# Optimization experiments

Hardware: AMD Instinct MI355X
Metric: run time of the kernel (lower is better)

Reference implementation:

```python
import jax, jax.numpy as jnp
import numpy as np

B = 131072   # batch
D = 16       # input_dim
L1 = 4       # num lattices in layer 1 (= ceil(D / DPL))
DPL = 4      # input_dim_per_lattice
E = 24       # output_size (ensemble columns)
K = 16       # calibrator keypoints per feature
NV = 2 ** DPL  # hypercube corners per lattice (lattice_keypoints=2 per dim)


def setup_inputs() -> dict:
    key = jax.random.key(0)
    k1, k2, k3, k4, k5 = jax.random.split(key, 5)
    x = jax.random.normal(k1, (B, D), jnp.float32)
    # piecewise-linear calibrators: sorted input keypoints, monotone outputs in [0,1]
    cal_kp = jnp.sort(jax.random.uniform(k2, (D, K), jnp.float32, -3.0, 3.0), axis=-1)
    raw = jax.random.uniform(k3, (D, K), jnp.float32, 0.1, 1.0)
    cv = jnp.cumsum(raw, axis=-1)
    cal_vals = (cv - cv[:, :1]) / (cv[:, -1:] - cv[:, :1])  # [D,K] in [0,1], increasing
    kernels1 = jax.random.uniform(k4, (E, L1, NV), jnp.float32)  # per-column layer-1 lattice vertices
    kernels2 = jax.random.uniform(k5, (E, 1, NV), jnp.float32)   # per-column layer-2 lattice vertices
    return {"x": x, "cal_kp": cal_kp, "cal_vals": cal_vals,
            "kernels1": kernels1, "kernels2": kernels2}


def _mlin_weights(xg):
    """Multilinear (HYPERCUBE) interpolation weights for unit lattices.
    xg: [..., L, d] with entries in [0,1]. Returns [..., L, 2^d] corner weights,
    corner index with dim 0 as most-significant bit."""
    d = xg.shape[-1]
    w = jnp.ones(xg.shape[:-1] + (1,), xg.dtype)
    for i in range(d):
        xi = xg[..., i]                              # [..., L]
        pair = jnp.stack([1.0 - xi, xi], axis=-1)    # [..., L, 2]
        w = (w[..., :, None] * pair[..., None, :]).reshape(*xg.shape[:-1], -1)
    return w


def reference(x, cal_kp, cal_vals, kernels1, kernels2):
    # 1) calibrate_and_stack: per-feature piecewise-linear calibration to [0,1]
    xc = jax.vmap(jnp.interp)(x.T, cal_kp, cal_vals).T           # [B, D]
    # 2) layer 1: split D dims into L1 lattices of DPL dims each (clip_inputs=True)
    xg1 = jnp.clip(xc.reshape(-1, L1, DPL), 0.0, 1.0)            # [B, L1, DPL]
    w1 = _mlin_weights(xg1)                                      # [B, L1, 2^DPL]
    h1 = jnp.einsum('blk,elk->ebl', w1, kernels1)                # [E, B, L1]
    # 3) layer 2: one lattice of DPL dims per ensemble column
    xg2 = jnp.clip(h1[:, :, None, :], 0.0, 1.0)                  # [E, B, 1, DPL]
    w2 = _mlin_weights(xg2)                                      # [E, B, 1, 2^DPL]
    out = jnp.einsum('eblk,elk->be', w2, kernels2)               # [B, E]
    return out
```

## Files before the change

### kernel.cpp

```cpp
#include <hip/hip_runtime.h>


typedef _Float16 f16x4 __attribute__((ext_vector_type(4)));
typedef float f32x4 __attribute__((ext_vector_type(4)));
typedef float f32x2 __attribute__((ext_vector_type(2)));

namespace {
constexpr int kD = 16, kE = 24, kK = 16, kNV = 16;
constexpr int kThreads = 256;
constexpr int kRPB = 64;
constexpr int kK2S = 20;
}

static __device__ __forceinline__ f32x2 fma2(f32x2 a, f32x2 b, f32x2 c) {
#if __has_builtin(__builtin_elementwise_fma)
    return __builtin_elementwise_fma(a, b, c);
#else
    return (f32x2){fmaf(a[0], b[0], c[0]), fmaf(a[1], b[1], c[1])};
#endif
}
static __device__ __forceinline__ f32x2 fma2s(f32x2 a, float b, float c) {
    return fma2(a, (f32x2){b, b}, (f32x2){c, c});
}
static __device__ __forceinline__ f32x2 clamp01(f32x2 v) {
#if __has_builtin(__builtin_elementwise_max) && __has_builtin(__builtin_elementwise_min)
    return __builtin_elementwise_min(
        __builtin_elementwise_max(v, (f32x2){0.f, 0.f}), (f32x2){1.f, 1.f});
#else
    return (f32x2){fminf(fmaxf(v[0], 0.f), 1.f), fminf(fmaxf(v[1], 0.f), 1.f)};
#endif
}

__global__ __launch_bounds__(kThreads, 5) void lattice_fwd(
    const float* __restrict__ x,
    const float* __restrict__ cal_kp,
    const float* __restrict__ cal_vals,
    const float* __restrict__ k1,
    const float* __restrict__ k2,
    float* __restrict__ out)
{
    __shared__ float sKp[kD * 16];
    __shared__ f32x4 sEnt[kD * 16];
    __shared__ f16x4 sW[4 * 4 * 64];
    __shared__ f16x4 sK1[4 * 2 * 64];
    __shared__ float sK2[32 * kK2S];

    const int tid  = threadIdx.x;
    const int lane = tid & 63;
    const int wv   = __builtin_amdgcn_readfirstlane(tid >> 6);
    const int q    = lane >> 4;
    const int r15  = lane & 15;

    const int rowBase = blockIdx.x * kRPB + wv * 16;

    f32x4 xin = *reinterpret_cast<const f32x4*>(
        x + (size_t)(rowBase + r15) * kD + 4 * q);

    sKp[tid] = ((tid & 15) == 15) ? __builtin_inff() : cal_kp[tid];
    if (tid < kD * 15) {
        int d = tid / 15;
        int k = tid - d * 15;
        float kp0 = cal_kp[d * kK + k];
        float kp1 = cal_kp[d * kK + k + 1];
        float v0  = cal_vals[d * kK + k];
        float v1  = cal_vals[d * kK + k + 1];
        float dxv = kp1 - kp0;
        float slope = (dxv > 0.0f) ? (v1 - v0) / dxv : 0.0f;
        sEnt[d * 16 + k] = (f32x4){kp0, slope, v0, 0.0f};
    }
    #pragma unroll
    for (int s0 = 0; s0 < 2; ++s0) {
        int s  = tid + s0 * kThreads;
        int l  = s >> 7;
        int n  = (s >> 6) & 1;
        int ls = s & 63;
        int e  = n * 16 + (ls & 15);
        int g  = ls >> 4;
        f16x4 v = {(_Float16)0.f, (_Float16)0.f, (_Float16)0.f, (_Float16)0.f};
        if (e < kE) {
            const float* src = k1 + ((size_t)(e * 4 + l) * kNV + 4 * g);
            v[0] = (_Float16)src[0]; v[1] = (_Float16)src[1];
            v[2] = (_Float16)src[2]; v[3] = (_Float16)src[3];
        }
        sK1[s] = v;
    }
    {
        int e = tid >> 3, j = tid & 7;
        float lo = 0.f, hi = 0.f;
        if (e < kE) { lo = k2[e * kNV + 2 * j]; hi = k2[e * kNV + 2 * j + 1]; }
        sK2[e * kK2S + j]     = lo;
        sK2[e * kK2S + 8 + j] = hi - lo;
    }

    __syncthreads();

    float xc[4];
    #pragma unroll
    for (int i = 0; i < 4; ++i) {
        const int d = 4 * q + i;
        const float xv = xin[i];
        const float* kpb = &sKp[d * 16];
        int j = 0;
        #pragma unroll
        for (int s = 8; s >= 1; s >>= 1) {
            float kps = kpb[j + s];
            j = (xv >= kps) ? j + s : j;
        }
        f32x4 ent = sEnt[d * 16 + j];
        float t = fmaf(ent[1], xv - ent[0], ent[2]);
        xc[i] = fminf(fmaxf(t, 0.0f), 1.0f);
    }

    float wf[16];
    {
        float a = xc[0], b = xc[1], c = xc[2], d = xc[3];
        float t2[2] = {1.0f - a, a};
        float t4[4];
        #pragma unroll
        for (int j = 0; j < 2; ++j) { t4[2*j] = t2[j]*(1.0f-b); t4[2*j+1] = t2[j]*b; }
        float t8[8];
        #pragma unroll
        for (int j = 0; j < 4; ++j) { t8[2*j] = t4[j]*(1.0f-c); t8[2*j+1] = t4[j]*c; }
        #pragma unroll
        for (int j = 0; j < 8; ++j) { wf[2*j] = t8[j]*(1.0f-d); wf[2*j+1] = t8[j]*d; }
    }

    #pragma unroll
    for (int g = 0; g < 4; ++g) {
        f16x4 v;
        v[0] = (_Float16)wf[4*g+0]; v[1] = (_Float16)wf[4*g+1];
        v[2] = (_Float16)wf[4*g+2]; v[3] = (_Float16)wf[4*g+3];
        sW[(wv * 4 + q) * 64 + r15 + 16 * g] = v;
    }
    asm volatile("s_waitcnt lgkmcnt(0)" ::: "memory");

    f16x4 af[4];
    #pragma unroll
    for (int l = 0; l < 4; ++l) af[l] = sW[(wv * 4 + l) * 64 + lane];

    #pragma unroll
    for (int n = 0; n < 2; ++n) {
        const int e = n * 16 + r15;

        f16x4 bf[4];
        #pragma unroll
        for (int l = 0; l < 4; ++l) bf[l] = sK1[(l * 2 + n) * 64 + lane];

        const float* kr = &sK2[e * kK2S];
        f32x4 ke0 = *reinterpret_cast<const f32x4*>(kr);
        f32x4 ke1 = *reinterpret_cast<const f32x4*>(kr + 4);
        f32x4 kd0 = *reinterpret_cast<const f32x4*>(kr + 8);
        f32x4 kd1 = *reinterpret_cast<const f32x4*>(kr + 12);
        float kbe[8] = {ke0[0],ke0[1],ke0[2],ke0[3], ke1[0],ke1[1],ke1[2],ke1[3]};
        float db [8] = {kd0[0],kd0[1],kd0[2],kd0[3], kd1[0],kd1[1],kd1[2],kd1[3]};

        f32x4 acc[4];
        #pragma unroll
        for (int l = 0; l < 4; ++l)
            acc[l] = __builtin_amdgcn_mfma_f32_16x16x16f16(
                af[l], bf[l], (f32x4){0.f, 0.f, 0.f, 0.f}, 0, 0, 0);

        #pragma unroll
        for (int p = 0; p < 2; ++p) {
            f32x2 h0 = clamp01((f32x2){acc[0][2*p], acc[0][2*p+1]});
            f32x2 h1 = clamp01((f32x2){acc[1][2*p], acc[1][2*p+1]});
            f32x2 h2 = clamp01((f32x2){acc[2][2*p], acc[2][2*p+1]});
            f32x2 h3 = clamp01((f32x2){acc[3][2*p], acc[3][2*p+1]});
            f32x2 v8[8];
            #pragma unroll
            for (int j = 0; j < 8; ++j) v8[j] = fma2s(h3, db[j], kbe[j]);
            f32x2 v4[4];
            #pragma unroll
            for (int j = 0; j < 4; ++j) v4[j] = fma2(h2, v8[2*j+1]-v8[2*j], v8[2*j]);
            f32x2 v2[2];
            #pragma unroll
            for (int j = 0; j < 2; ++j) v2[j] = fma2(h1, v4[2*j+1]-v4[2*j], v4[2*j]);
            f32x2 o = fma2(h0, v2[1]-v2[0], v2[0]);
            if (e < kE) {
                size_t r0 = (size_t)(rowBase + q * 4 + 2 * p);
                out[r0 * kE + e]       = o[0];
                out[(r0 + 1) * kE + e] = o[1];
            }
        }
    }
}

extern "C" void kernel_launch(void* const* d_in, const int* in_sizes, int n_in,
                              void* d_out, int out_size, void* d_ws, size_t ws_size,
                              hipStream_t stream) {
    const float* x        = (const float*)d_in[0];
    const float* cal_kp   = (const float*)d_in[1];
    const float* cal_vals = (const float*)d_in[2];
    const float* k1       = (const float*)d_in[3];
    const float* k2       = (const float*)d_in[4];
    float* out = (float*)d_out;

    hipLaunchKernelGGL(lattice_fwd, dim3(131072 / kRPB), dim3(kThreads), 0, stream,
                       x, cal_kp, cal_vals, k1, k2, out);
}
```

Baseline: 14.23 us.

## Pad shared arrays, precompute calibrator affine terms, and reorder layer-2 evaluation to cut registers

Pads the shared keypoint, calibration and weight arrays to odd strides so LDS accesses hit fewer bank conflicts. Each calibrator segment is stored as a slope/intercept pair, so the lookup needs one FMA and a smaller LDS read. The layer-2 kernel table is interleaved and consumed four entries at a time, streaming K2 loads instead of holding all 16 values. Launch bounds go from 5 to 8 blocks per SM, which caps register use to raise occupancy and may cause spills.

```diff
diff --git a/kernel.cpp b/kernel.cpp
--- a/kernel.cpp
+++ b/kernel.cpp
@@ -9,7 +9,10 @@
 constexpr int kD = 16, kE = 24, kK = 16, kNV = 16;
 constexpr int kThreads = 256;
 constexpr int kRPB = 64;
-constexpr int kK2S = 20;
+constexpr int kKpS  = 17;
+constexpr int kAffS = 17;
+constexpr int kWS   = 67;
+constexpr int kK2S  = 20;
 }
 
 static __device__ __forceinline__ f32x2 fma2(f32x2 a, f32x2 b, f32x2 c) {
@@ -23,15 +26,10 @@
     return fma2(a, (f32x2){b, b}, (f32x2){c, c});
 }
 static __device__ __forceinline__ f32x2 clamp01(f32x2 v) {
-#if __has_builtin(__builtin_elementwise_max) && __has_builtin(__builtin_elementwise_min)
-    return __builtin_elementwise_min(
-        __builtin_elementwise_max(v, (f32x2){0.f, 0.f}), (f32x2){1.f, 1.f});
-#else
     return (f32x2){fminf(fmaxf(v[0], 0.f), 1.f), fminf(fmaxf(v[1], 0.f), 1.f)};
-#endif
-}
-
-__global__ __launch_bounds__(kThreads, 5) void lattice_fwd(
+}
+
+__global__ __launch_bounds__(kThreads, 8) void lattice_fwd(
     const float* __restrict__ x,
     const float* __restrict__ cal_kp,
     const float* __restrict__ cal_vals,
@@ -39,9 +37,9 @@
     const float* __restrict__ k2,
     float* __restrict__ out)
 {
-    __shared__ float sKp[kD * 16];
-    __shared__ f32x4 sEnt[kD * 16];
-    __shared__ f16x4 sW[4 * 4 * 64];
+    __shared__ float sKp[kD * kKpS];
+    __shared__ f32x2 sAff[kD * kAffS];
+    __shared__ f16x4 sW[16 * kWS];
     __shared__ f16x4 sK1[4 * 2 * 64];
     __shared__ float sK2[32 * kK2S];
 
@@ -56,7 +54,10 @@
     f32x4 xin = *reinterpret_cast<const f32x4*>(
         x + (size_t)(rowBase + r15) * kD + 4 * q);
 
-    sKp[tid] = ((tid & 15) == 15) ? __builtin_inff() : cal_kp[tid];
+    {
+        int d = tid >> 4, k = tid & 15;
+        sKp[d * kKpS + k] = (k == 15) ? __builtin_inff() : cal_kp[tid];
+    }
     if (tid < kD * 15) {
         int d = tid / 15;
         int k = tid - d * 15;
@@ -66,7 +67,7 @@
         float v1  = cal_vals[d * kK + k + 1];
         float dxv = kp1 - kp0;
         float slope = (dxv > 0.0f) ? (v1 - v0) / dxv : 0.0f;
-        sEnt[d * 16 + k] = (f32x4){kp0, slope, v0, 0.0f};
+        sAff[d * kAffS + k] = (f32x2){slope, fmaf(-slope, kp0, v0)};
     }
     #pragma unroll
     for (int s0 = 0; s0 < 2; ++s0) {
@@ -85,11 +86,14 @@
         sK1[s] = v;
     }
     {
-        int e = tid >> 3, j = tid & 7;
-        float lo = 0.f, hi = 0.f;
-        if (e < kE) { lo = k2[e * kNV + 2 * j]; hi = k2[e * kNV + 2 * j + 1]; }
-        sK2[e * kK2S + j]     = lo;
-        sK2[e * kK2S + 8 + j] = hi - lo;
+        int e = tid >> 3, j4 = (tid >> 1) & 3, h = tid & 1;
+        float a = 0.f, d = 0.f;
+        if (e < kE) {
+            a = k2[e * kNV + 4 * j4 + 2 * h];
+            d = k2[e * kNV + 4 * j4 + 2 * h + 1] - a;
+        }
+        sK2[e * kK2S + 4 * j4 + h]     = a;
+        sK2[e * kK2S + 4 * j4 + 2 + h] = d;
     }
 
     __syncthreads();
@@ -99,16 +103,15 @@
     for (int i = 0; i < 4; ++i) {
         const int d = 4 * q + i;
         const float xv = xin[i];
-        const float* kpb = &sKp[d * 16];
+        const float* kpb = &sKp[d * kKpS];
         int j = 0;
         #pragma unroll
         for (int s = 8; s >= 1; s >>= 1) {
             float kps = kpb[j + s];
             j = (xv >= kps) ? j + s : j;
         }
-        f32x4 ent = sEnt[d * 16 + j];
-        float t = fmaf(ent[1], xv - ent[0], ent[2]);
-        xc[i] = fminf(fmaxf(t, 0.0f), 1.0f);
+        f32x2 ent = sAff[d * kAffS + j];
+        xc[i] = fminf(fmaxf(fmaf(ent[0], xv, ent[1]), 0.0f), 1.0f);
     }
 
     float wf[16];
@@ -130,52 +133,52 @@
         f16x4 v;
         v[0] = (_Float16)wf[4*g+0]; v[1] = (_Float16)wf[4*g+1];
         v[2] = (_Float16)wf[4*g+2]; v[3] = (_Float16)wf[4*g+3];
-        sW[(wv * 4 + q) * 64 + r15 + 16 * g] = v;
+        sW[(wv * 4 + q) * kWS + r15 + 16 * g] = v;
     }
     asm volatile("s_waitcnt lgkmcnt(0)" ::: "memory");
 
     f16x4 af[4];
     #pragma unroll
-    for (int l = 0; l < 4; ++l) af[l] = sW[(wv * 4 + l) * 64 + lane];
+    for (int l = 0; l < 4; ++l) af[l] = sW[(wv * 4 + l) * kWS + lane];
 
     #pragma unroll
     for (int n = 0; n < 2; ++n) {
         const int e = n * 16 + r15;
 
-        f16x4 bf[4];
-        #pragma unroll
-        for (int l = 0; l < 4; ++l) bf[l] = sK1[(l * 2 + n) * 64 + lane];
-
+        f32x4 acc[4];
+        #pragma unroll
+        for (int l = 0; l < 4; ++l) {
+            f16x4 bf = sK1[(l * 2 + n) * 64 + lane];
+            acc[l] = __builtin_amdgcn_mfma_f32_16x16x16f16(
+                af[l], bf, (f32x4){0.f, 0.f, 0.f, 0.f}, 0, 0, 0);
+        }
+
+        f32x2 h3a = clamp01((f32x2){acc[3][0], acc[3][1]});
+        f32x2 h3b = clamp01((f32x2){acc[3][2], acc[3][3]});
+        f32x2 h2a = clamp01((f32x2){acc[2][0], acc[2][1]});
+        f32x2 h2b = clamp01((f32x2){acc[2][2], acc[2][3]});
+
+        f32x2 v4a[4], v4b[4];
         const float* kr = &sK2[e * kK2S];
-        f32x4 ke0 = *reinterpret_cast<const f32x4*>(kr);
-        f32x4 ke1 = *reinterpret_cast<const f32x4*>(kr + 4);
-        f32x4 kd0 = *reinterpret_cast<const f32x4*>(kr + 8);
-        f32x4 kd1 = *reinterpret_cast<const f32x4*>(kr + 12);
-        float kbe[8] = {ke0[0],ke0[1],ke0[2],ke0[3], ke1[0],ke1[1],ke1[2],ke1[3]};
-        float db [8] = {kd0[0],kd0[1],kd0[2],kd0[3], kd1[0],kd1[1],kd1[2],kd1[3]};
-
-        f32x4 acc[4];
-        #pragma unroll
-        for (int l = 0; l < 4; ++l)
-            acc[l] = __builtin_amdgcn_mfma_f32_16x16x16f16(
-                af[l], bf[l], (f32x4){0.f, 0.f, 0.f, 0.f}, 0, 0, 0);
+        #pragma unroll
+        for (int j4 = 0; j4 < 4; ++j4) {
+            f32x4 kq = *reinterpret_cast<const f32x4*>(kr + 4 * j4);
+            f32x2 a0 = fma2s(h3a, kq[2], kq[0]);
+            f32x2 b0 = fma2s(h3a, kq[3], kq[1]);
+            v4a[j4]  = fma2(h2a, b0 - a0, a0);
+            f32x2 a1 = fma2s(h3b, kq[2], kq[0]);
+            f32x2 b1 = fma2s(h3b, kq[3], kq[1]);
+            v4b[j4]  = fma2(h2b, b1 - a1, a1);
+        }
 
         #pragma unroll
         for (int p = 0; p < 2; ++p) {
+            f32x2 h1 = clamp01((f32x2){acc[1][2*p], acc[1][2*p+1]});
             f32x2 h0 = clamp01((f32x2){acc[0][2*p], acc[0][2*p+1]});
-            f32x2 h1 = clamp01((f32x2){acc[1][2*p], acc[1][2*p+1]});
-            f32x2 h2 = clamp01((f32x2){acc[2][2*p], acc[2][2*p+1]});
-            f32x2 h3 = clamp01((f32x2){acc[3][2*p], acc[3][2*p+1]});
-            f32x2 v8[8];
-            #pragma unroll
-            for (int j = 0; j < 8; ++j) v8[j] = fma2s(h3, db[j], kbe[j]);
-            f32x2 v4[4];
-            #pragma unroll
-            for (int j = 0; j < 4; ++j) v4[j] = fma2(h2, v8[2*j+1]-v8[2*j], v8[2*j]);
-            f32x2 v2[2];
-            #pragma unroll
-            for (int j = 0; j < 2; ++j) v2[j] = fma2(h1, v4[2*j+1]-v4[2*j], v4[2*j]);
-            f32x2 o = fma2(h0, v2[1]-v2[0], v2[0]);
+            const f32x2* v4 = (p == 0) ? v4a : v4b;
+            f32x2 w0 = fma2(h1, v4[1] - v4[0], v4[0]);
+            f32x2 w1 = fma2(h1, v4[3] - v4[2], v4[2]);
+            f32x2 o  = fma2(h0, w1 - w0, w0);
             if (e < kE) {
                 size_t r0 = (size_t)(rowBase + q * 4 + 2 * p);
                 out[r0 * kE + e]       = o[0];
```

Result: no change. 14.13 us (-0.7%).
